# Kernel optimization log

Hardware: AMD Instinct MI355X
Metric: run time of the kernel (lower is better)

The kernel has to match this reference:

```python
import jax, jax.numpy as jnp
import numpy as np
import math

N_HEAD = 16
N_EMBED = 1024
BLOCK_SIZE = 2048


def setup_inputs() -> dict:
    key = jax.random.key(0)
    k0, k1, k2, k3, k4 = jax.random.split(key, 5)
    B, T, C = 2, 2048, N_EMBED
    x = jax.random.normal(k0, (B, T, C), dtype=jnp.float32)
    # torch nn.Linear weights: [out_features, in_features]
    s_attn = 1.0 / math.sqrt(C)
    W_attn = jax.random.uniform(k1, (3 * C, C), dtype=jnp.float32, minval=-s_attn, maxval=s_attn)
    b_attn = jax.random.uniform(k2, (3 * C,), dtype=jnp.float32, minval=-s_attn, maxval=s_attn)
    W_proj = jax.random.uniform(k3, (C, C), dtype=jnp.float32, minval=-s_attn, maxval=s_attn)
    b_proj = jax.random.uniform(k4, (C,), dtype=jnp.float32, minval=-s_attn, maxval=s_attn)
    return {"x": x, "W_attn": W_attn, "b_attn": b_attn, "W_proj": W_proj, "b_proj": b_proj}


def reference(x, W_attn, b_attn, W_proj, b_proj):
    B, T, C = x.shape
    H = N_HEAD
    D = C // H
    qkv = x @ W_attn.T + b_attn                     # [B,T,3C]
    q, k, v = jnp.split(qkv, 3, axis=2)
    # [B,T,C] -> [B,H,T,D]
    q = q.reshape(B, T, H, D).transpose(0, 2, 1, 3)
    k = k.reshape(B, T, H, D).transpose(0, 2, 1, 3)
    v = v.reshape(B, T, H, D).transpose(0, 2, 1, 3)
    scale = 1.0 / math.sqrt(D)
    attn = jnp.einsum('bhqd,bhkd->bhqk', q, k) * scale   # [B,H,T,T]
    causal = jnp.tril(jnp.ones((T, T), dtype=bool))
    attn = jnp.where(causal[None, None, :, :], attn, -jnp.inf)
    attn = jax.nn.softmax(attn, axis=-1)
    y = jnp.einsum('bhqk,bhkd->bhqd', attn, v)           # [B,H,T,D]
    y = y.transpose(0, 2, 1, 3).reshape(B, T, C)
    return y @ W_proj.T + b_proj
```

## Files before the change

### kernel.cpp

```cpp
#include <hip/hip_runtime.h>
#include <hip/hip_bf16.h>

#define B_  2
#define T_  2048
#define C_  1024
#define H_  16
#define D_  64
#define M_  (B_*T_)
#define N1_ (3*C_)

typedef short bf16x8 __attribute__((ext_vector_type(8)));
typedef short bf16x4 __attribute__((ext_vector_type(4)));
typedef float f32x4 __attribute__((ext_vector_type(4)));
typedef unsigned short u16;
typedef u16 u16x8 __attribute__((ext_vector_type(8)));

#define QSCALE 0.18033688011112042f
#define C8     11.541560327111707f

__device__ __forceinline__ u16 f2bf(float f) {
  unsigned u = __float_as_uint(f);
  u += 0x7FFFu + ((u >> 16) & 1u);
  return (u16)(u >> 16);
}

__device__ __forceinline__ void gload16(const void* g, void* l) {
  __builtin_amdgcn_global_load_lds((__attribute__((address_space(1))) void*)g,
                                   (__attribute__((address_space(3))) void*)l,
                                   16, 0, 0);
}

__global__ __launch_bounds__(256) void cvt3(const float* __restrict__ x,
                                            const float* __restrict__ wa,
                                            const float* __restrict__ wp,
                                            u16* __restrict__ out) {
  int i = (blockIdx.x * 256 + threadIdx.x) * 8;
  const float* src;
  int off;
  if (i < M_ * C_)                 { src = x;  off = 0; }
  else if (i < M_ * C_ + N1_ * C_) { src = wa; off = M_ * C_; }
  else                             { src = wp; off = M_ * C_ + N1_ * C_; }
  float4 a = *(const float4*)(src + (i - off));
  float4 b = *(const float4*)(src + (i - off) + 4);
  u16x8 o;
  o[0] = f2bf(a.x); o[1] = f2bf(a.y); o[2] = f2bf(a.z); o[3] = f2bf(a.w);
  o[4] = f2bf(b.x); o[5] = f2bf(b.y); o[6] = f2bf(b.z); o[7] = f2bf(b.w);
  *(u16x8*)(out + i) = o;
}

__device__ __forceinline__ void gemm_core(const u16* __restrict__ A,
                                          const u16* __restrict__ W,
                                          u16* As, u16* Bs,
                                          f32x4 (&acc)[4][4],
                                          int m0, int n0, int K) {
  int tid = threadIdx.x;
  int lane = tid & 63, wid = tid >> 6;
  int wr = wid >> 1, wc = wid & 1;

  int arow = wid * 16 + (lane >> 2);
  int ag = lane & 3;
  int sg = ag ^ ((arow >> 1) & 3);
  const u16* aSrc0 = A + (m0 + arow) * K + sg * 8;
  const u16* aSrc1 = aSrc0 + 64 * K;
  const u16* bSrc0 = W + (n0 + arow) * K + sg * 8;
  const u16* bSrc1 = bSrc0 + 64 * K;
  u16* aDst0 = As + (wid * 16) * 32;
  u16* aDst1 = As + (64 + wid * 16) * 32;
  u16* bDst0 = Bs + (wid * 16) * 32;
  u16* bDst1 = Bs + (64 + wid * 16) * 32;

  int rg = lane >> 4;
  int aoff[4], boff[4];
#pragma unroll
  for (int m = 0; m < 4; ++m) {
    int row = wr * 64 + m * 16 + (lane & 15);
    aoff[m] = row * 32 + (rg ^ ((row >> 1) & 3)) * 8;
    row = wc * 64 + m * 16 + (lane & 15);
    boff[m] = row * 32 + (rg ^ ((row >> 1) & 3)) * 8;
  }

  for (int kt = 0; kt < K / 32; ++kt) {
    int k0 = kt * 32;
    __syncthreads();
    gload16(aSrc0 + k0, aDst0);
    gload16(aSrc1 + k0, aDst1);
    gload16(bSrc0 + k0, bDst0);
    gload16(bSrc1 + k0, bDst1);
    __syncthreads();

    bf16x8 af[4], bfr[4];
#pragma unroll
    for (int m = 0; m < 4; ++m) af[m] = *(const bf16x8*)(As + aoff[m]);
#pragma unroll
    for (int n = 0; n < 4; ++n) bfr[n] = *(const bf16x8*)(Bs + boff[n]);
#pragma unroll
    for (int m = 0; m < 4; ++m)
#pragma unroll
      for (int n = 0; n < 4; ++n)
        acc[m][n] = __builtin_amdgcn_mfma_f32_16x16x32_bf16(af[m], bfr[n], acc[m][n], 0, 0, 0);
  }
}

__global__ __launch_bounds__(256) void gemm_qkv(const u16* __restrict__ A,
                                                const u16* __restrict__ W,
                                                const float* __restrict__ bias,
                                                u16* __restrict__ Qb,
                                                u16* __restrict__ Kb,
                                                u16* __restrict__ Vt) {
  __shared__ __align__(16) u16 As[128 * 32];
  __shared__ __align__(16) u16 Bs[128 * 32];
  f32x4 acc[4][4] = {};
  int m0 = blockIdx.x * 128, n0 = blockIdx.y * 128;
  gemm_core(A, W, As, Bs, acc, m0, n0, C_);

  int lane = threadIdx.x & 63, wid = threadIdx.x >> 6;
  int wr = wid >> 1, wc = wid & 1;
  int rg = lane >> 4, cl = lane & 15;
#pragma unroll
  for (int n = 0; n < 4; ++n) {
    int gn = n0 + wc * 64 + n * 16 + cl;
    float bv = bias[gn];
    int seg = gn >> 10, cc = gn & 1023;
    int h = cc >> 6, d = cc & 63;
    float sc = (seg == 0) ? QSCALE : 1.0f;
#pragma unroll
    for (int m = 0; m < 4; ++m) {
#pragma unroll
      for (int r = 0; r < 4; ++r) {
        int gm = m0 + wr * 64 + m * 16 + rg * 4 + r;
        int b = gm >> 11, t = gm & 2047;
        u16 val = f2bf((acc[m][n][r] + bv) * sc);
        int bh = b * 16 + h;
        if (seg == 0)      Qb[(bh * 2048 + t) * 64 + d] = val;
        else if (seg == 1) Kb[(bh * 2048 + t) * 64 + d] = val;
        else               Vt[(bh * 64 + d) * 2048 + t] = val;
      }
    }
  }
}

__global__ __launch_bounds__(256) void gemm_proj(const u16* __restrict__ A,
                                                 const u16* __restrict__ W,
                                                 const float* __restrict__ bias,
                                                 float* __restrict__ out) {
  __shared__ __align__(16) u16 As[128 * 32];
  __shared__ __align__(16) u16 Bs[128 * 32];
  f32x4 acc[4][4] = {};
  int m0 = blockIdx.x * 128, n0 = blockIdx.y * 128;
  gemm_core(A, W, As, Bs, acc, m0, n0, C_);

  int lane = threadIdx.x & 63, wid = threadIdx.x >> 6;
  int wr = wid >> 1, wc = wid & 1;
  int rg = lane >> 4, cl = lane & 15;
#pragma unroll
  for (int n = 0; n < 4; ++n) {
    int gn = n0 + wc * 64 + n * 16 + cl;
    float bv = bias[gn];
#pragma unroll
    for (int m = 0; m < 4; ++m) {
#pragma unroll
      for (int r = 0; r < 4; ++r) {
        int gm = m0 + wr * 64 + m * 16 + rg * 4 + r;
        out[gm * 1024 + gn] = acc[m][n][r] + bv;
      }
    }
  }
}

__global__ __launch_bounds__(128, 2) void attn_fwd(const u16* __restrict__ Qb,
                                                   const u16* __restrict__ Kb,
                                                   const u16* __restrict__ Vt,
                                                   u16* __restrict__ Yb) {
  __shared__ __align__(16) u16 Ps[2][2][32 * 64];
  __shared__ __align__(16) f32x4 Co[8][64];
  __shared__ float Cl[2][64];
  int tid = threadIdx.x, lane = tid & 63, wid = tid >> 6;
  int cl = lane & 15, kg = lane >> 4;
  int bid = blockIdx.x;
  int bh = bid & 31;
  int qwi = 63 - (bid >> 5);
  int qw0 = qwi * 32;
  int jmax = qwi >> 1;
  int fc0 = wid * 2;
  const u16* Qp = Qb + (size_t)bh * (2048 * 64);
  const u16* Kp = Kb + (size_t)bh * (2048 * 64);
  const u16* Vp = Vt + (size_t)bh * (64 * 2048);
  u16* P0 = Ps[wid][0];
  u16* P1 = Ps[wid][1];

  int kbase = cl * 64 + kg * 8 + fc0 * 1024;
  int vbase = cl * 2048 + wid * 32 + kg * 8;

  bf16x8 qf[2][2];
#pragma unroll
  for (int fr = 0; fr < 2; ++fr)
#pragma unroll
    for (int dk = 0; dk < 2; ++dk)
      qf[fr][dk] = *(const bf16x8*)(Qp + (qw0 + fr * 16 + cl) * 64 + dk * 32 + kg * 8);

  f32x4 o[2][4] = {};
  float lsum[2] = {0.f, 0.f};
  const f32x4 CINIT = {-C8, -C8, -C8, -C8};

  auto LOADK = [&](bf16x8 (&kf)[2][2], int j) {
    const u16* Kj = Kp + j * 4096 + kbase;
#pragma unroll
    for (int fcl = 0; fcl < 2; ++fcl) {
      kf[fcl][0] = *(const bf16x8*)(Kj + fcl * 1024);
      kf[fcl][1] = *(const bf16x8*)(Kj + fcl * 1024 + 32);
    }
  };

  auto LOADV = [&](bf16x8 (&vf)[4], int j) {
    const u16* Vj = Vp + j * 64 + vbase;
#pragma unroll
    for (int dc = 0; dc < 4; ++dc)
      vf[dc] = *(const bf16x8*)(Vj + dc * 32768);
  };

  auto SEXP = [&](bf16x8 (&kf)[2][2], int j, bool edge, u16* Pw) {
    f32x4 s[2][2];
#pragma unroll
    for (int fcl = 0; fcl < 2; ++fcl)
#pragma unroll
      for (int fr = 0; fr < 2; ++fr) {
        f32x4 z = CINIT;
        z = __builtin_amdgcn_mfma_f32_16x16x32_bf16(kf[fcl][0], qf[fr][0], z, 0, 0, 0);
        z = __builtin_amdgcn_mfma_f32_16x16x32_bf16(kf[fcl][1], qf[fr][1], z, 0, 0, 0);
        s[fr][fcl] = z;
      }
    if (edge) {
#pragma unroll
      for (int fr = 0; fr < 2; ++fr) {
        int qg = qw0 + fr * 16 + cl;
#pragma unroll
        for (int fcl = 0; fcl < 2; ++fcl)
#pragma unroll
          for (int r = 0; r < 4; ++r)
            if (j * 64 + (fc0 + fcl) * 16 + kg * 4 + r > qg) s[fr][fcl][r] = -1e30f;
      }
    }
#pragma unroll
    for (int fr = 0; fr < 2; ++fr) {
      int rowb = (fr * 16 + cl) * 64;
#pragma unroll
      for (int fcl = 0; fcl < 2; ++fcl) {
        float p0 = exp2f(s[fr][fcl][0]);
        float p1 = exp2f(s[fr][fcl][1]);
        float p2 = exp2f(s[fr][fcl][2]);
        float p3 = exp2f(s[fr][fcl][3]);
        lsum[fr] += (p0 + p1) + (p2 + p3);
        union { bf16x4 v; __hip_bfloat162 h[2]; } pk;
        pk.h[0] = __float22bfloat162_rn(make_float2(p0, p1));
        pk.h[1] = __float22bfloat162_rn(make_float2(p2, p3));
        int fc = fc0 + fcl;
        *(bf16x4*)(Pw + rowb + (((fc * 2 + (kg >> 1)) ^ (cl & 7)) * 8) + (kg & 1) * 4) = pk.v;
      }
    }
  };

  auto PV = [&](bf16x8 (&vf)[4], u16* Pw) {
#pragma unroll
    for (int fr = 0; fr < 2; ++fr) {
      int rowb = (fr * 16 + cl) * 64;
      bf16x8 pf = *(const bf16x8*)(Pw + rowb + (((wid * 4 + kg) ^ (cl & 7)) * 8));
#pragma unroll
      for (int dc = 0; dc < 4; ++dc)
        o[fr][dc] = __builtin_amdgcn_mfma_f32_16x16x32_bf16(pf, vf[dc], o[fr][dc], 0, 0, 0);
    }
  };

  bool edgeMine = (fc0 <= ((qwi & 1) ? 3 : 1));

  bf16x8 k0[2][2], k1[2][2], v0[4], v1[4];
  LOADK(k0, 0);
  if (jmax >= 1) LOADK(k1, 1);

  int j = 0;
  while (j + 1 < jmax) {
    LOADV(v0, j);
    LOADV(v1, j + 1);
    SEXP(k0, j, false, P0);
    SEXP(k1, j + 1, false, P1);
    LOADK(k0, j + 2);
    LOADK(k1, (j + 3 <= jmax) ? j + 3 : jmax);
    PV(v0, P0);
    PV(v1, P1);
    j += 2;
  }
  if (j == jmax) {
    if (edgeMine) { LOADV(v0, j); SEXP(k0, j, true, P0); PV(v0, P0); }
  } else {
    LOADV(v0, j);
    SEXP(k0, j, false, P0);
    if (edgeMine) { LOADV(v1, j + 1); SEXP(k1, j + 1, true, P1); }
    PV(v0, P0);
    if (edgeMine) PV(v1, P1);
  }

  if (wid == 1) {
#pragma unroll
    for (int fr = 0; fr < 2; ++fr) {
      Cl[fr][lane] = lsum[fr];
#pragma unroll
      for (int dc = 0; dc < 4; ++dc) Co[fr * 4 + dc][lane] = o[fr][dc];
    }
  }
  __syncthreads();
  if (wid == 0) {
    int b = bh >> 4, h = bh & 15;
#pragma unroll
    for (int fr = 0; fr < 2; ++fr) {
      float l = lsum[fr] + Cl[fr][lane];
#pragma unroll
      for (int dc = 0; dc < 4; ++dc) o[fr][dc] += Co[fr * 4 + dc][lane];
      l += __shfl_xor(l, 16);
      l += __shfl_xor(l, 32);
      float linv = 1.f / l;
      float li[4];
#pragma unroll
      for (int r = 0; r < 4; ++r) li[r] = __shfl(linv, kg * 4 + r);
#pragma unroll
      for (int dc = 0; dc < 4; ++dc)
#pragma unroll
        for (int r = 0; r < 4; ++r) {
          int t = qw0 + fr * 16 + kg * 4 + r;
          int d = dc * 16 + cl;
          Yb[((size_t)(b * 2048 + t)) * 1024 + h * 64 + d] = f2bf(o[fr][dc][r] * li[r]);
        }
    }
  }
}

extern "C" void kernel_launch(void* const* d_in, const int* in_sizes, int n_in,
                              void* d_out, int out_size, void* d_ws, size_t ws_size,
                              hipStream_t stream) {
  const float* x  = (const float*)d_in[0];
  const float* Wa = (const float*)d_in[1];
  const float* ba = (const float*)d_in[2];
  const float* Wp = (const float*)d_in[3];
  const float* bp = (const float*)d_in[4];
  float* out = (float*)d_out;

  u16* xb  = (u16*)d_ws;
  u16* Wab = xb  + (size_t)M_ * C_;
  u16* Wpb = Wab + (size_t)N1_ * C_;
  u16* Qb  = Wpb + (size_t)C_ * C_;
  u16* Kb  = Qb  + (size_t)M_ * C_;
  u16* Vt  = Kb  + (size_t)M_ * C_;
  u16* Yb  = Vt  + (size_t)M_ * C_;

  cvt3<<<(M_ * C_ + N1_ * C_ + C_ * C_) / 2048, 256, 0, stream>>>(x, Wa, Wp, xb);
  gemm_qkv<<<dim3(M_ / 128, N1_ / 128), 256, 0, stream>>>(xb, Wab, ba, Qb, Kb, Vt);
  attn_fwd<<<2048, 128, 0, stream>>>(Qb, Kb, Vt, Yb);
  gemm_proj<<<dim3(M_ / 128, C_ / 128), 256, 0, stream>>>(Yb, Wpb, bp, out);
}
```

Baseline: 136.8 us.

## Deepen attention KV pipeline with double-buffered V registers and reuse P smem for reduction

Reworks the attention inner loop to process four KV blocks per iteration, using two extra V register sets so V loads are issued one step ahead alongside the K prefetch. The intent is to hide global-load latency for V behind the softmax and PV MFMAs. The cross-wave reduction buffers now alias the P shared-memory tiles after an extra barrier. This lowers LDS use per block, but the extra vector registers may push against the two-blocks-per-CU launch bound and cause spills.

```diff
diff --git a/kernel.cpp b/kernel.cpp
--- a/kernel.cpp
+++ b/kernel.cpp
@@ -172,8 +172,6 @@
                                                    const u16* __restrict__ Vt,
                                                    u16* __restrict__ Yb) {
   __shared__ __align__(16) u16 Ps[2][2][32 * 64];
-  __shared__ __align__(16) f32x4 Co[8][64];
-  __shared__ float Cl[2][64];
   int tid = threadIdx.x, lane = tid & 63, wid = tid >> 6;
   int cl = lane & 15, kg = lane >> 4;
   int bid = blockIdx.x;
@@ -272,38 +270,63 @@
 
   bool edgeMine = (fc0 <= ((qwi & 1) ? 3 : 1));
 
-  bf16x8 k0[2][2], k1[2][2], v0[4], v1[4];
-  LOADK(k0, 0);
-  if (jmax >= 1) LOADK(k1, 1);
-
+  bf16x8 k0[2][2], k1[2][2], v0[4], v1[4], v2[4], v3[4];
   int j = 0;
-  while (j + 1 < jmax) {
-    LOADV(v0, j);
-    LOADV(v1, j + 1);
+  LOADK(k0, 0); LOADV(v0, 0);
+  if (jmax >= 1) { LOADK(k1, 1); LOADV(v1, 1); }
+
+  while (j + 3 < jmax) {
+    LOADV(v2, j + 2); LOADV(v3, j + 3);
+    SEXP(k0, j, false, P0);
+    SEXP(k1, j + 1, false, P1);
+    LOADK(k0, j + 2); LOADK(k1, j + 3);
+    PV(v0, P0); PV(v1, P1);
+
+    int n0 = (j + 4 <= jmax) ? j + 4 : jmax;
+    int n1 = (j + 5 <= jmax) ? j + 5 : jmax;
+    LOADV(v0, n0); LOADV(v1, n1);
+    SEXP(k0, j + 2, false, P0);
+    SEXP(k1, j + 3, false, P1);
+    LOADK(k0, n0); LOADK(k1, n1);
+    PV(v2, P0); PV(v3, P1);
+    j += 4;
+  }
+  int r = jmax - j + 1;
+  if (r == 1) {
+    if (edgeMine) { SEXP(k0, j, true, P0); PV(v0, P0); }
+  } else if (r == 2) {
+    SEXP(k0, j, false, P0);
+    if (edgeMine) SEXP(k1, j + 1, true, P1);
+    PV(v0, P0);
+    if (edgeMine) PV(v1, P1);
+  } else if (r == 3) {
+    LOADV(v2, j + 2);
     SEXP(k0, j, false, P0);
     SEXP(k1, j + 1, false, P1);
     LOADK(k0, j + 2);
-    LOADK(k1, (j + 3 <= jmax) ? j + 3 : jmax);
-    PV(v0, P0);
-    PV(v1, P1);
-    j += 2;
-  }
-  if (j == jmax) {
-    if (edgeMine) { LOADV(v0, j); SEXP(k0, j, true, P0); PV(v0, P0); }
+    PV(v0, P0); PV(v1, P1);
+    if (edgeMine) { SEXP(k0, j + 2, true, P0); PV(v2, P0); }
   } else {
-    LOADV(v0, j);
+    LOADV(v2, j + 2); LOADV(v3, j + 3);
     SEXP(k0, j, false, P0);
-    if (edgeMine) { LOADV(v1, j + 1); SEXP(k1, j + 1, true, P1); }
-    PV(v0, P0);
-    if (edgeMine) PV(v1, P1);
-  }
-
+    SEXP(k1, j + 1, false, P1);
+    LOADK(k0, j + 2); LOADK(k1, j + 3);
+    PV(v0, P0); PV(v1, P1);
+    SEXP(k0, j + 2, false, P0);
+    if (edgeMine) SEXP(k1, j + 3, true, P1);
+    PV(v2, P0);
+    if (edgeMine) PV(v3, P1);
+  }
+
+  __syncthreads();
+  f32x4* Co = (f32x4*)&Ps[0][0][0];
+  float*  Cl = (float*)&Ps[1][0][0];
   if (wid == 1) {
 #pragma unroll
     for (int fr = 0; fr < 2; ++fr) {
-      Cl[fr][lane] = lsum[fr];
-#pragma unroll
-      for (int dc = 0; dc < 4; ++dc) Co[fr * 4 + dc][lane] = o[fr][dc];
+      Cl[fr * 64 + lane] = lsum[fr];
+#pragma unroll
+      for (int dc = 0; dc < 4; ++dc) Co[(fr * 4 + dc) * 64 + lane] = o[fr][dc];
     }
   }
   __syncthreads();
@@ -311,22 +334,22 @@
     int b = bh >> 4, h = bh & 15;
 #pragma unroll
     for (int fr = 0; fr < 2; ++fr) {
-      float l = lsum[fr] + Cl[fr][lane];
-#pragma unroll
-      for (int dc = 0; dc < 4; ++dc) o[fr][dc] += Co[fr * 4 + dc][lane];
+      float l = lsum[fr] + Cl[fr * 64 + lane];
+#pragma unroll
+      for (int dc = 0; dc < 4; ++dc) o[fr][dc] += Co[(fr * 4 + dc) * 64 + lane];
       l += __shfl_xor(l, 16);
       l += __shfl_xor(l, 32);
       float linv = 1.f / l;
       float li[4];
 #pragma unroll
-      for (int r = 0; r < 4; ++r) li[r] = __shfl(linv, kg * 4 + r);
+      for (int r2 = 0; r2 < 4; ++r2) li[r2] = __shfl(linv, kg * 4 + r2);
 #pragma unroll
       for (int dc = 0; dc < 4; ++dc)
 #pragma unroll
-        for (int r = 0; r < 4; ++r) {
-          int t = qw0 + fr * 16 + kg * 4 + r;
+        for (int r2 = 0; r2 < 4; ++r2) {
+          int t = qw0 + fr * 16 + kg * 4 + r2;
           int d = dc * 16 + cl;
-          Yb[((size_t)(b * 2048 + t)) * 1024 + h * 64 + d] = f2bf(o[fr][dc][r] * li[r]);
+          Yb[((size_t)(b * 2048 + t)) * 1024 + h * 64 + d] = f2bf(o[fr][dc][r2] * li[r2]);
         }
     }
   }
```

Result: no change. 135.9 us (-0.6%).
